# Performance work log

Hardware: AMD Instinct MI355X
Metric: run time of the kernel (lower is better)

## Reference

```python
import jax, jax.numpy as jnp
import numpy as np

NUM_HEADS = 16
HEAD_DIM = 64
D_MODEL = 1024
B, L = 8, 4096


def _relative_position_encoding(seq_len, dim):
    positions = jnp.arange(seq_len, dtype=jnp.float32)[:, None]
    div_term = jnp.exp(jnp.arange(0, dim, 2, dtype=jnp.float32) * (-(np.log(10000.0) / dim)))
    ang = positions * div_term  # [L, dim//2]
    pe = jnp.zeros((seq_len, dim), dtype=jnp.float32)
    pe = pe.at[:, 0::2].set(jnp.sin(ang))
    pe = pe.at[:, 1::2].set(jnp.cos(ang))
    return pe


def setup_inputs() -> dict:
    key = jax.random.key(0)
    k1, k2, k3 = jax.random.split(key, 3)
    x = jax.random.normal(k1, (B, L, D_MODEL), dtype=jnp.float32)
    w_qkv = jax.random.normal(k2, (D_MODEL, 3 * NUM_HEADS * HEAD_DIM), dtype=jnp.float32) * (1.0 / np.sqrt(D_MODEL))
    b_qkv = jnp.zeros((3 * NUM_HEADS * HEAD_DIM,), dtype=jnp.float32)
    w_out = jax.random.normal(k3, (NUM_HEADS * HEAD_DIM, D_MODEL), dtype=jnp.float32) * (1.0 / np.sqrt(NUM_HEADS * HEAD_DIM))
    b_out = jnp.zeros((D_MODEL,), dtype=jnp.float32)
    return {"x": x, "w_qkv": w_qkv, "b_qkv": b_qkv, "w_out": w_out, "b_out": b_out}


def reference(x, w_qkv, b_qkv, w_out, b_out):
    Bq, Lq, _ = x.shape
    qkv = x @ w_qkv + b_qkv                              # [B, L, 3*H*Dh]
    qkv = qkv.reshape(Bq, Lq, NUM_HEADS, 3 * HEAD_DIM)   # [B, L, H, 3*Dh]
    q, k, v = jnp.split(qkv, 3, axis=-1)                 # each [B, L, H, Dh]
    pos_enc = _relative_position_encoding(Lq, HEAD_DIM)  # [L, Dh]
    k = k + pos_enc[None, :, None, :]
    scale = jnp.sqrt(jnp.float32(HEAD_DIM))
    # NOTE: faithful to source -- contraction over head_dim with batch dims (B, L):
    # attention matrix is [B, L, H, H] (across heads, not sequence).
    attn = jnp.einsum('blhd,bl gd->blhg'.replace(' ', ''), q, k) / scale  # [B, L, H, H]
    attn = jax.nn.softmax(attn, axis=-1)
    out = jnp.einsum('blhg,blgd->blhd', attn, v)          # [B, L, H, Dh]
    out = out.reshape(Bq, Lq, NUM_HEADS * HEAD_DIM)
    return out @ w_out + b_out
```

## Files before the change

### kernel.cpp

```cpp
#include <hip/hip_runtime.h>
#include <hip/hip_bf16.h>
#include <cstdint>
#include <cstddef>

#define NH   16
#define DHD  64
#define DM   1024
#define BSZ  8
#define SEQ  4096
#define NTOK (BSZ*SEQ)
#define NQKV (3*NH*DHD)

typedef __attribute__((ext_vector_type(8))) __bf16 bf16x8;
typedef __attribute__((ext_vector_type(4))) float  floatx4;

static __device__ __forceinline__ unsigned short f2bf(float f) {
    unsigned int u = __float_as_uint(f);
    u += 0x7fffu + ((u >> 16) & 1u);
    return (unsigned short)(u >> 16);
}
static __device__ __forceinline__ float bf2f(unsigned int us) {
    return __uint_as_float(us << 16);
}
static __device__ __forceinline__ void load_lds16(const void* g, void* l) {
    __builtin_amdgcn_global_load_lds((__attribute__((address_space(1))) void*)g,
                                     (__attribute__((address_space(3))) void*)l,
                                     16, 0, 0);
}

__global__ __launch_bounds__(256) void k_cast_bf16(const float* __restrict__ in,
                                                   unsigned short* __restrict__ out, int n4) {
    int i = blockIdx.x * 256 + threadIdx.x;
    if (i >= n4) return;
    float4 v = ((const float4*)in)[i];
    ushort4 o;
    o.x = f2bf(v.x); o.y = f2bf(v.y); o.z = f2bf(v.z); o.w = f2bf(v.w);
    ((ushort4*)out)[i] = o;
}

template<int R, int C>
__global__ __launch_bounds__(256) void k_transpose_cast(const float* __restrict__ in,
                                                        unsigned short* __restrict__ out) {
    __shared__ float tile[32][33];
    int tx = threadIdx.x, ty = threadIdx.y;
    int col = blockIdx.x * 32 + tx;
#pragma unroll
    for (int k = 0; k < 4; k++) {
        int row = blockIdx.y * 32 + ty + k * 8;
        tile[ty + k * 8][tx] = in[(size_t)row * C + col];
    }
    __syncthreads();
#pragma unroll
    for (int k = 0; k < 4; k++) {
        int ocol = blockIdx.x * 32 + ty + k * 8;
        int orow = blockIdx.y * 32 + tx;
        out[(size_t)ocol * R + orow] = f2bf(tile[tx][ty + k * 8]);
    }
}

__global__ __launch_bounds__(256) void k_pe(float* __restrict__ pe) {
    int t = blockIdx.x * 256 + threadIdx.x;
    int l = t >> 5, i = t & 31;
    float dv = expf(-0.14391156831212787f * (float)(2 * i));
    float ang = (float)l * dv;
    pe[l * 64 + 2 * i]     = sinf(ang);
    pe[l * 64 + 2 * i + 1] = cosf(ang);
}

template<int N, int EPI>
__global__ __launch_bounds__(256) void k_gemm(const unsigned short* __restrict__ A,
                                              const unsigned short* __restrict__ BT,
                                              const float* __restrict__ bias,
                                              const float* __restrict__ pe,
                                              void* __restrict__ Cout) {
    constexpr int K = 1024;
    __shared__ __align__(16) short lds[8192];
    short* As = lds;
    short* Bs = lds + 4096;

    int tid  = threadIdx.x;
    int lane = tid & 63;
    int wid  = tid >> 6;
    int m0 = blockIdx.y * 128;
    int n0 = blockIdx.x * 128;
    int wr = wid >> 1, wc = wid & 1;
    int l15 = lane & 15;
    int kq  = (lane >> 4) * 8;

    floatx4 acc[4][4];
#pragma unroll
    for (int i = 0; i < 4; i++)
#pragma unroll
        for (int j = 0; j < 4; j++) acc[i][j] = (floatx4){0.f, 0.f, 0.f, 0.f};

    int ci0 = wid * 128 + lane;
    int ci1 = ci0 + 64;
    const unsigned short* pa0 = A  + (size_t)(m0 + (ci0 >> 2)) * K + (ci0 & 3) * 8;
    const unsigned short* pa1 = A  + (size_t)(m0 + (ci1 >> 2)) * K + (ci1 & 3) * 8;
    const unsigned short* pb0 = BT + (size_t)(n0 + (ci0 >> 2)) * K + (ci0 & 3) * 8;
    const unsigned short* pb1 = BT + (size_t)(n0 + (ci1 >> 2)) * K + (ci1 & 3) * 8;
    short* la0 = As + ci0 * 8;
    short* la1 = As + ci1 * 8;
    short* lb0 = Bs + ci0 * 8;
    short* lb1 = Bs + ci1 * 8;

    for (int kb = 0; kb < K; kb += 32) {
        __syncthreads();
        load_lds16(pa0 + kb, la0);
        load_lds16(pa1 + kb, la1);
        load_lds16(pb0 + kb, lb0);
        load_lds16(pb1 + kb, lb1);
        __syncthreads();

        bf16x8 aF[4], bF[4];
#pragma unroll
        for (int i = 0; i < 4; i++)
            aF[i] = *(const bf16x8*)&As[(wr * 64 + i * 16 + l15) * 32 + kq];
#pragma unroll
        for (int j = 0; j < 4; j++)
            bF[j] = *(const bf16x8*)&Bs[(wc * 64 + j * 16 + l15) * 32 + kq];
#pragma unroll
        for (int i = 0; i < 4; i++)
#pragma unroll
            for (int j = 0; j < 4; j++)
                acc[i][j] = __builtin_amdgcn_mfma_f32_16x16x32_bf16(aF[i], bF[j], acc[i][j], 0, 0, 0);
    }

    int rbase = (lane >> 4) * 4;
#pragma unroll
    for (int j = 0; j < 4; j++) {
        int col = n0 + wc * 64 + j * 16 + l15;
        float bv = bias[col];
        int h = 0, rc = 0;
        if (EPI == 1) { h = col / 192; rc = col - h * 192; }
#pragma unroll
        for (int i = 0; i < 4; i++) {
#pragma unroll
            for (int r = 0; r < 4; r++) {
                int row = m0 + wr * 64 + i * 16 + rbase + r;
                float v = acc[i][j][r] + bv;
                if (EPI == 1) {
                    if (rc < 64)        v *= 0.125f;
                    else if (rc < 128)  v += pe[(row & (SEQ - 1)) * 64 + (rc - 64)];
                    ((unsigned short*)Cout)[(size_t)row * N + col] = f2bf(v);
                } else {
                    ((float*)Cout)[(size_t)row * N + col] = v;
                }
            }
        }
    }
}

__global__ __launch_bounds__(256) void k_attn(const unsigned short* __restrict__ qkv,
                                              unsigned short* __restrict__ aout) {
    __shared__ __align__(16) float X4[4][3264];
    __shared__ float S4[4][272];
    int tid = threadIdx.x, wid = tid >> 6, lane = tid & 63;
    int t = blockIdx.x * 4 + wid;

    float* X = X4[wid];
    const unsigned short* src = qkv + (size_t)t * NQKV;

#pragma unroll
    for (int c = 0; c < 6; c++) {
        int ci = c * 64 + lane;
        uint4 u = ((const uint4*)src)[ci];
        int j0 = ci * 8;
        int h  = j0 / 192;
        int rc = j0 - h * 192;
        float* dst = X + h * 204 + rc;
        floatx4 f0 = { bf2f(u.x & 0xffff), bf2f(u.x >> 16), bf2f(u.y & 0xffff), bf2f(u.y >> 16) };
        floatx4 f1 = { bf2f(u.z & 0xffff), bf2f(u.z >> 16), bf2f(u.w & 0xffff), bf2f(u.w >> 16) };
        *(floatx4*)dst       = f0;
        *(floatx4*)(dst + 4) = f1;
    }
    __syncthreads();

    int h  = lane >> 2;
    int g0 = (lane & 3) * 4;
    const float* Q = X + h * 204;
    float s0 = 0.f, s1 = 0.f, s2 = 0.f, s3 = 0.f;
#pragma unroll 8
    for (int d = 0; d < 64; d++) {
        float qd = Q[d];
        s0 += qd * X[(g0 + 0) * 204 + 64 + d];
        s1 += qd * X[(g0 + 1) * 204 + 64 + d];
        s2 += qd * X[(g0 + 2) * 204 + 64 + d];
        s3 += qd * X[(g0 + 3) * 204 + 64 + d];
    }
    float mx = fmaxf(fmaxf(s0, s1), fmaxf(s2, s3));
    mx = fmaxf(mx, __shfl_xor(mx, 1));
    mx = fmaxf(mx, __shfl_xor(mx, 2));
    float e0 = __expf(s0 - mx), e1 = __expf(s1 - mx), e2 = __expf(s2 - mx), e3 = __expf(s3 - mx);
    float sum = e0 + e1 + e2 + e3;
    sum += __shfl_xor(sum, 1);
    sum += __shfl_xor(sum, 2);
    float inv = 1.0f / sum;
    float* Sr = &S4[wid][h * 17];
    Sr[g0 + 0] = e0 * inv; Sr[g0 + 1] = e1 * inv; Sr[g0 + 2] = e2 * inv; Sr[g0 + 3] = e3 * inv;
    __syncthreads();

    int db = lane & 3;
    floatx4 o0 = {0,0,0,0}, o1 = {0,0,0,0}, o2 = {0,0,0,0}, o3 = {0,0,0,0};
    const float* Sh = &S4[wid][h * 17];
#pragma unroll
    for (int g = 0; g < 16; g++) {
        float p = Sh[g];
        const floatx4* Vg = (const floatx4*)(X + g * 204 + 128 + db * 16);
        o0 += Vg[0] * p;
        o1 += Vg[1] * p;
        o2 += Vg[2] * p;
        o3 += Vg[3] * p;
    }
    unsigned int w[8];
    w[0] = (unsigned)f2bf(o0[0]) | ((unsigned)f2bf(o0[1]) << 16);
    w[1] = (unsigned)f2bf(o0[2]) | ((unsigned)f2bf(o0[3]) << 16);
    w[2] = (unsigned)f2bf(o1[0]) | ((unsigned)f2bf(o1[1]) << 16);
    w[3] = (unsigned)f2bf(o1[2]) | ((unsigned)f2bf(o1[3]) << 16);
    w[4] = (unsigned)f2bf(o2[0]) | ((unsigned)f2bf(o2[1]) << 16);
    w[5] = (unsigned)f2bf(o2[2]) | ((unsigned)f2bf(o2[3]) << 16);
    w[6] = (unsigned)f2bf(o3[0]) | ((unsigned)f2bf(o3[1]) << 16);
    w[7] = (unsigned)f2bf(o3[2]) | ((unsigned)f2bf(o3[3]) << 16);
    uint4* dst = (uint4*)&aout[(size_t)t * DM + h * 64 + db * 16];
    dst[0] = make_uint4(w[0], w[1], w[2], w[3]);
    dst[1] = make_uint4(w[4], w[5], w[6], w[7]);
}

extern "C" void kernel_launch(void* const* d_in, const int* in_sizes, int n_in,
                              void* d_out, int out_size, void* d_ws, size_t ws_size,
                              hipStream_t stream) {
    const float* x     = (const float*)d_in[0];
    const float* w_qkv = (const float*)d_in[1];
    const float* b_qkv = (const float*)d_in[2];
    const float* w_out = (const float*)d_in[3];
    const float* b_out = (const float*)d_in[4];
    float* out = (float*)d_out;

    char* ws = (char*)d_ws;
    float*          pe    = (float*)ws;
    unsigned short* wqkvT = (unsigned short*)(ws + (1u << 20));
    unsigned short* woutT = (unsigned short*)(ws + (1u << 20) + 6291456u);
    unsigned short* xbf   = (unsigned short*)(ws + (1u << 20) + 6291456u + 2097152u);
    unsigned short* qkv   = (unsigned short*)(ws + (1u << 20) + 6291456u + 2097152u + 67108864u);
    unsigned short* aout  = xbf;

    k_cast_bf16<<<(NTOK * DM / 4 + 255) / 256, 256, 0, stream>>>(x, xbf, NTOK * DM / 4);
    k_transpose_cast<1024, 3072><<<dim3(96, 32), dim3(32, 8), 0, stream>>>(w_qkv, wqkvT);
    k_transpose_cast<1024, 1024><<<dim3(32, 32), dim3(32, 8), 0, stream>>>(w_out, woutT);
    k_pe<<<512, 256, 0, stream>>>(pe);

    k_gemm<NQKV, 1><<<dim3(NQKV / 128, NTOK / 128), 256, 0, stream>>>(xbf, wqkvT, b_qkv, pe, qkv);

    k_attn<<<NTOK / 4, 256, 0, stream>>>(qkv, aout);

    k_gemm<DM, 0><<<dim3(DM / 128, NTOK / 128), 256, 0, stream>>>(aout, woutT, b_out, nullptr, out);
}
```

Measured before the change: 730.6 us.

## Replace GEMM with 256x256 8-wave pipelined MFMA kernel with swizzled LDS

Replaces the simple 128x128 single-buffered GEMM with a 256x256-tile, 512-thread kernel. It double-buffers K=64 tiles in LDS through async global-to-LDS loads interleaved with MFMA phases, and uses priority boosts and explicit waitcnt/barriers. It also adds an XOR-swizzled LDS layout against bank conflicts, an XCD-aware block-index remap, and an epilogue staged through LDS so global stores are vectorized. The goal is to hide memory latency and raise MFMA utilization in both projection GEMMs, at the cost of 128KB of LDS per block, fragile hand scheduling and lower occupancy.

```diff
diff --git a/kernel.cpp b/kernel.cpp
--- a/kernel.cpp
+++ b/kernel.cpp
@@ -68,84 +68,237 @@
 }
 
 template<int N, int EPI>
-__global__ __launch_bounds__(256) void k_gemm(const unsigned short* __restrict__ A,
-                                              const unsigned short* __restrict__ BT,
-                                              const float* __restrict__ bias,
-                                              const float* __restrict__ pe,
-                                              void* __restrict__ Cout) {
-    constexpr int K = 1024;
-    __shared__ __align__(16) short lds[8192];
-    short* As = lds;
-    short* Bs = lds + 4096;
-
-    int tid  = threadIdx.x;
-    int lane = tid & 63;
-    int wid  = tid >> 6;
-    int m0 = blockIdx.y * 128;
-    int n0 = blockIdx.x * 128;
-    int wr = wid >> 1, wc = wid & 1;
-    int l15 = lane & 15;
-    int kq  = (lane >> 4) * 8;
-
-    floatx4 acc[4][4];
-#pragma unroll
-    for (int i = 0; i < 4; i++)
-#pragma unroll
-        for (int j = 0; j < 4; j++) acc[i][j] = (floatx4){0.f, 0.f, 0.f, 0.f};
-
-    int ci0 = wid * 128 + lane;
-    int ci1 = ci0 + 64;
-    const unsigned short* pa0 = A  + (size_t)(m0 + (ci0 >> 2)) * K + (ci0 & 3) * 8;
-    const unsigned short* pa1 = A  + (size_t)(m0 + (ci1 >> 2)) * K + (ci1 & 3) * 8;
-    const unsigned short* pb0 = BT + (size_t)(n0 + (ci0 >> 2)) * K + (ci0 & 3) * 8;
-    const unsigned short* pb1 = BT + (size_t)(n0 + (ci1 >> 2)) * K + (ci1 & 3) * 8;
-    short* la0 = As + ci0 * 8;
-    short* la1 = As + ci1 * 8;
-    short* lb0 = Bs + ci0 * 8;
-    short* lb1 = Bs + ci1 * 8;
-
-    for (int kb = 0; kb < K; kb += 32) {
-        __syncthreads();
-        load_lds16(pa0 + kb, la0);
-        load_lds16(pa1 + kb, la1);
-        load_lds16(pb0 + kb, lb0);
-        load_lds16(pb1 + kb, lb1);
-        __syncthreads();
-
-        bf16x8 aF[4], bF[4];
-#pragma unroll
-        for (int i = 0; i < 4; i++)
-            aF[i] = *(const bf16x8*)&As[(wr * 64 + i * 16 + l15) * 32 + kq];
-#pragma unroll
-        for (int j = 0; j < 4; j++)
-            bF[j] = *(const bf16x8*)&Bs[(wc * 64 + j * 16 + l15) * 32 + kq];
-#pragma unroll
-        for (int i = 0; i < 4; i++)
-#pragma unroll
-            for (int j = 0; j < 4; j++)
-                acc[i][j] = __builtin_amdgcn_mfma_f32_16x16x32_bf16(aF[i], bF[j], acc[i][j], 0, 0, 0);
-    }
-
-    int rbase = (lane >> 4) * 4;
-#pragma unroll
-    for (int j = 0; j < 4; j++) {
-        int col = n0 + wc * 64 + j * 16 + l15;
-        float bv = bias[col];
-        int h = 0, rc = 0;
-        if (EPI == 1) { h = col / 192; rc = col - h * 192; }
-#pragma unroll
-        for (int i = 0; i < 4; i++) {
-#pragma unroll
-            for (int r = 0; r < 4; r++) {
-                int row = m0 + wr * 64 + i * 16 + rbase + r;
-                float v = acc[i][j][r] + bv;
-                if (EPI == 1) {
-                    if (rc < 64)        v *= 0.125f;
-                    else if (rc < 128)  v += pe[(row & (SEQ - 1)) * 64 + (rc - 64)];
-                    ((unsigned short*)Cout)[(size_t)row * N + col] = f2bf(v);
-                } else {
-                    ((float*)Cout)[(size_t)row * N + col] = v;
+__global__ __launch_bounds__(512, 2) void k_gemm8(const unsigned short* __restrict__ A,
+                                                  const unsigned short* __restrict__ BT,
+                                                  const float* __restrict__ bias,
+                                                  const float* __restrict__ pe,
+                                                  void* __restrict__ Cout) {
+    constexpr int K   = 1024;
+    constexpr int NKT = K / 64;
+    constexpr int NIT = NKT / 2;
+    constexpr int NBX = N / 256;
+    constexpr int nwg = NBX * (NTOK / 256);
+
+    __shared__ __align__(16) short sh[65536];
+    char* shb = (char*)sh;
+
+    const int tid  = threadIdx.x;
+    const int lane = tid & 63;
+    const int wid  = tid >> 6;
+    const int l15  = lane & 15;
+    const int q4   = lane >> 4;
+    const int wr   = wid >> 2;
+    const int wc   = wid & 3;
+
+    const int id = blockIdx.x;
+    const int sw = (id & 7) * (nwg >> 3) + (id >> 3);
+    const int m0 = (sw / NBX) * 256;
+    const int n0 = (sw % NBX) * 256;
+
+    int cj[2];
+    const unsigned short* srcA[2];
+    const unsigned short* srcB[2];
+#pragma unroll
+    for (int j = 0; j < 2; j++) {
+        int c  = wid * 128 + j * 64 + lane;
+        cj[j]  = c;
+        int rh = c >> 3;
+        int sl = (c & 7) ^ (rh & 7);
+        srcA[j] = A  + (size_t)(m0 + rh) * K + sl * 8;
+        srcB[j] = BT + (size_t)(n0 + rh) * K + sl * 8;
+    }
+    auto STAGE_A = [&](int kt, int half) {
+#pragma unroll
+        for (int j = 0; j < 2; j++)
+            load_lds16(srcA[j] + half * 128 * K + kt * 64,
+                       shb + (kt & 1) * 32768 + half * 16384 + cj[j] * 16);
+    };
+    auto STAGE_B = [&](int kt, int half) {
+#pragma unroll
+        for (int j = 0; j < 2; j++)
+            load_lds16(srcB[j] + half * 128 * K + kt * 64,
+                       shb + 65536 + (kt & 1) * 32768 + half * 16384 + cj[j] * 16);
+    };
+
+    const int swz  = (l15 & 7) << 4;
+    const int cb0  = ((q4 * 16) ^ swz);
+    const int cb1  = ((64 + q4 * 16) ^ swz);
+    const int rowA = (wr * 128 + l15) * 128;
+    const int rowB = (wc * 64  + l15) * 128;
+    auto RDA = [&](int b, int i, int cb) -> bf16x8 {
+        return *(const bf16x8*)(shb + b * 32768 + rowA + i * 2048 + cb);
+    };
+    auto RDB = [&](int b, int n, int cb) -> bf16x8 {
+        return *(const bf16x8*)(shb + 65536 + b * 32768 + rowB + n * 2048 + cb);
+    };
+
+    floatx4 acc[8][4];
+#pragma unroll
+    for (int i = 0; i < 8; i++)
+#pragma unroll
+        for (int n = 0; n < 4; n++) acc[i][n] = (floatx4){0.f, 0.f, 0.f, 0.f};
+
+    bf16x8 aF0[4][2], aF1[4][2], bF[4][2];
+
+    STAGE_A(0, 0); STAGE_B(0, 0); STAGE_A(0, 1); STAGE_B(0, 1);
+    STAGE_A(1, 0); STAGE_B(1, 0);
+    asm volatile("s_waitcnt vmcnt(4)" ::: "memory");
+    __builtin_amdgcn_s_barrier();
+
+#pragma unroll 1
+    for (int it = 0; it < NIT; ++it) {
+        const int kB = 2 * it + 1;
+        const bool more = (it < NIT - 1);
+
+#pragma unroll
+        for (int i = 0; i < 4; i++) { aF0[i][0] = RDA(0, i, cb0); aF0[i][1] = RDA(0, i, cb1); }
+#pragma unroll
+        for (int n = 0; n < 4; n++) bF[n][0] = RDB(0, n, cb0);
+        STAGE_A(kB, 1);
+        __builtin_amdgcn_s_barrier();
+        asm volatile("s_waitcnt lgkmcnt(0)" ::: "memory");
+        __builtin_amdgcn_s_setprio(1);
+#pragma unroll
+        for (int i = 0; i < 4; i++)
+#pragma unroll
+            for (int n = 0; n < 4; n++)
+                acc[i][n] = __builtin_amdgcn_mfma_f32_16x16x32_bf16(aF0[i][0], bF[n][0], acc[i][n], 0, 0, 0);
+        __builtin_amdgcn_s_setprio(0);
+        __builtin_amdgcn_s_barrier();
+
+#pragma unroll
+        for (int i = 0; i < 4; i++) { aF1[i][0] = RDA(0, i + 4, cb0); aF1[i][1] = RDA(0, i + 4, cb1); }
+#pragma unroll
+        for (int n = 0; n < 4; n++) bF[n][1] = RDB(0, n, cb1);
+        STAGE_B(kB, 1);
+        __builtin_amdgcn_s_barrier();
+        asm volatile("s_waitcnt lgkmcnt(0)" ::: "memory");
+        __builtin_amdgcn_s_setprio(1);
+#pragma unroll
+        for (int i = 0; i < 4; i++)
+#pragma unroll
+            for (int n = 0; n < 4; n++)
+                acc[i][n] = __builtin_amdgcn_mfma_f32_16x16x32_bf16(aF0[i][1], bF[n][1], acc[i][n], 0, 0, 0);
+        __builtin_amdgcn_s_setprio(0);
+        __builtin_amdgcn_s_barrier();
+
+        if (more) STAGE_A(kB + 1, 0);
+        __builtin_amdgcn_s_barrier();
+        __builtin_amdgcn_s_setprio(1);
+#pragma unroll
+        for (int i = 0; i < 4; i++)
+#pragma unroll
+            for (int n = 0; n < 4; n++)
+                acc[i + 4][n] = __builtin_amdgcn_mfma_f32_16x16x32_bf16(aF1[i][0], bF[n][0], acc[i + 4][n], 0, 0, 0);
+        __builtin_amdgcn_s_setprio(0);
+        __builtin_amdgcn_s_barrier();
+
+        if (more) STAGE_B(kB + 1, 0);
+        if (more) asm volatile("s_waitcnt vmcnt(4)" ::: "memory");
+        else      asm volatile("s_waitcnt vmcnt(0)" ::: "memory");
+        __builtin_amdgcn_s_barrier();
+        __builtin_amdgcn_s_setprio(1);
+#pragma unroll
+        for (int i = 0; i < 4; i++)
+#pragma unroll
+            for (int n = 0; n < 4; n++)
+                acc[i + 4][n] = __builtin_amdgcn_mfma_f32_16x16x32_bf16(aF1[i][1], bF[n][1], acc[i + 4][n], 0, 0, 0);
+        __builtin_amdgcn_s_setprio(0);
+        __builtin_amdgcn_s_barrier();
+
+#pragma unroll
+        for (int i = 0; i < 4; i++) { aF0[i][0] = RDA(1, i, cb0); aF0[i][1] = RDA(1, i, cb1); }
+#pragma unroll
+        for (int n = 0; n < 4; n++) bF[n][0] = RDB(1, n, cb0);
+        if (more) STAGE_A(kB + 1, 1);
+        __builtin_amdgcn_s_barrier();
+        asm volatile("s_waitcnt lgkmcnt(0)" ::: "memory");
+        __builtin_amdgcn_s_setprio(1);
+#pragma unroll
+        for (int i = 0; i < 4; i++)
+#pragma unroll
+            for (int n = 0; n < 4; n++)
+                acc[i][n] = __builtin_amdgcn_mfma_f32_16x16x32_bf16(aF0[i][0], bF[n][0], acc[i][n], 0, 0, 0);
+        __builtin_amdgcn_s_setprio(0);
+        __builtin_amdgcn_s_barrier();
+
+#pragma unroll
+        for (int i = 0; i < 4; i++) { aF1[i][0] = RDA(1, i + 4, cb0); aF1[i][1] = RDA(1, i + 4, cb1); }
+#pragma unroll
+        for (int n = 0; n < 4; n++) bF[n][1] = RDB(1, n, cb1);
+        if (more) STAGE_B(kB + 1, 1);
+        __builtin_amdgcn_s_barrier();
+        asm volatile("s_waitcnt lgkmcnt(0)" ::: "memory");
+        __builtin_amdgcn_s_setprio(1);
+#pragma unroll
+        for (int i = 0; i < 4; i++)
+#pragma unroll
+            for (int n = 0; n < 4; n++)
+                acc[i][n] = __builtin_amdgcn_mfma_f32_16x16x32_bf16(aF0[i][1], bF[n][1], acc[i][n], 0, 0, 0);
+        __builtin_amdgcn_s_setprio(0);
+        __builtin_amdgcn_s_barrier();
+
+        if (more) STAGE_A(kB + 2, 0);
+        __builtin_amdgcn_s_barrier();
+        __builtin_amdgcn_s_setprio(1);
+#pragma unroll
+        for (int i = 0; i < 4; i++)
+#pragma unroll
+            for (int n = 0; n < 4; n++)
+                acc[i + 4][n] = __builtin_amdgcn_mfma_f32_16x16x32_bf16(aF1[i][0], bF[n][0], acc[i + 4][n], 0, 0, 0);
+        __builtin_amdgcn_s_setprio(0);
+        __builtin_amdgcn_s_barrier();
+
+        if (more) STAGE_B(kB + 2, 0);
+        if (more) asm volatile("s_waitcnt vmcnt(4)" ::: "memory");
+        __builtin_amdgcn_s_barrier();
+        __builtin_amdgcn_s_setprio(1);
+#pragma unroll
+        for (int i = 0; i < 4; i++)
+#pragma unroll
+            for (int n = 0; n < 4; n++)
+                acc[i + 4][n] = __builtin_amdgcn_mfma_f32_16x16x32_bf16(aF1[i][1], bF[n][1], acc[i + 4][n], 0, 0, 0);
+        __builtin_amdgcn_s_setprio(0);
+        __builtin_amdgcn_s_barrier();
+    }
+
+    float* X = (float*)shb + wid * 2176;
+#pragma unroll
+    for (int cidx = 0; cidx < 4; ++cidx) {
+#pragma unroll
+        for (int i2 = 0; i2 < 2; ++i2) {
+            const int i = cidx * 2 + i2;
+#pragma unroll
+            for (int n = 0; n < 4; ++n) {
+                const int col = n0 + wc * 64 + n * 16 + l15;
+                const float bv = bias[col];
+                int rc = 0;
+                if (EPI == 1) { int h = col / 192; rc = col - h * 192; }
+#pragma unroll
+                for (int r = 0; r < 4; ++r) {
+                    const int lrow = i2 * 16 + q4 * 4 + r;
+                    float v = acc[i][n][r] + bv;
+                    if (EPI == 1) {
+                        const int grow = m0 + wr * 128 + cidx * 32 + lrow;
+                        if (rc < 64)        v *= 0.125f;
+                        else if (rc < 128)  v += pe[(grow & (SEQ - 1)) * 64 + (rc - 64)];
+                    }
+                    X[lrow * 68 + n * 16 + l15] = v;
                 }
+            }
+        }
+#pragma unroll
+        for (int rr = 0; rr < 8; ++rr) {
+            const int lr   = rr * 4 + q4;
+            const int grow = m0 + wr * 128 + cidx * 32 + lr;
+            const float* p = X + lr * 68 + l15 * 4;
+            if (EPI == 1) {
+                ushort4 o;
+                o.x = f2bf(p[0]); o.y = f2bf(p[1]); o.z = f2bf(p[2]); o.w = f2bf(p[3]);
+                *(ushort4*)((unsigned short*)Cout + (size_t)grow * N + n0 + wc * 64 + l15 * 4) = o;
+            } else {
+                float4 o = make_float4(p[0], p[1], p[2], p[3]);
+                *(float4*)((float*)Cout + (size_t)grow * N + n0 + wc * 64 + l15 * 4) = o;
             }
         }
     }
@@ -249,9 +402,9 @@
     k_transpose_cast<1024, 1024><<<dim3(32, 32), dim3(32, 8), 0, stream>>>(w_out, woutT);
     k_pe<<<512, 256, 0, stream>>>(pe);
 
-    k_gemm<NQKV, 1><<<dim3(NQKV / 128, NTOK / 128), 256, 0, stream>>>(xbf, wqkvT, b_qkv, pe, qkv);
+    k_gemm8<NQKV, 1><<<dim3((NQKV / 256) * (NTOK / 256)), 512, 0, stream>>>(xbf, wqkvT, b_qkv, pe, qkv);
 
     k_attn<<<NTOK / 4, 256, 0, stream>>>(qkv, aout);
 
-    k_gemm<DM, 0><<<dim3(DM / 128, NTOK / 128), 256, 0, stream>>>(aout, woutT, b_out, nullptr, out);
-}
+    k_gemm8<DM, 0><<<dim3((DM / 256) * (NTOK / 256)), 512, 0, stream>>>(aout, woutT, b_out, nullptr, out);
+}
```

Measured after the change: 874.5 us. 1.2x slower.

## Deepen GEMM K-tile to 64 with XOR-swizzled LDS and staged coalesced epilogue

Applied to the files above, without the earlier changes.

The bf16 MFMA GEMM now stages 64-wide K slices per iteration, halving the number of barrier pairs, and applies an XOR swizzle to the LDS layout to avoid bank conflicts on fragment reads. The epilogue writes accumulators through a per-wave LDS staging buffer so each lane stores 4 contiguous outputs as vector stores instead of scattered scalar stores. This doubles the LDS footprint to 32KB, which may reduce occupancy, and adds an extra barrier and LDS round trip in the epilogue.

```diff
diff --git a/kernel.cpp b/kernel.cpp
--- a/kernel.cpp
+++ b/kernel.cpp
@@ -74,18 +74,17 @@
                                               const float* __restrict__ pe,
                                               void* __restrict__ Cout) {
     constexpr int K = 1024;
-    __shared__ __align__(16) short lds[8192];
-    short* As = lds;
-    short* Bs = lds + 4096;
-
-    int tid  = threadIdx.x;
-    int lane = tid & 63;
-    int wid  = tid >> 6;
-    int m0 = blockIdx.y * 128;
-    int n0 = blockIdx.x * 128;
-    int wr = wid >> 1, wc = wid & 1;
-    int l15 = lane & 15;
-    int kq  = (lane >> 4) * 8;
+    __shared__ __align__(16) short lds[16384];
+    char* shb = (char*)lds;
+
+    const int tid  = threadIdx.x;
+    const int lane = tid & 63;
+    const int wid  = tid >> 6;
+    const int l15  = lane & 15;
+    const int q4   = lane >> 4;
+    const int m0 = blockIdx.y * 128;
+    const int n0 = blockIdx.x * 128;
+    const int wr = wid >> 1, wc = wid & 1;
 
     floatx4 acc[4][4];
 #pragma unroll
@@ -93,59 +92,87 @@
 #pragma unroll
         for (int j = 0; j < 4; j++) acc[i][j] = (floatx4){0.f, 0.f, 0.f, 0.f};
 
-    int ci0 = wid * 128 + lane;
-    int ci1 = ci0 + 64;
-    const unsigned short* pa0 = A  + (size_t)(m0 + (ci0 >> 2)) * K + (ci0 & 3) * 8;
-    const unsigned short* pa1 = A  + (size_t)(m0 + (ci1 >> 2)) * K + (ci1 & 3) * 8;
-    const unsigned short* pb0 = BT + (size_t)(n0 + (ci0 >> 2)) * K + (ci0 & 3) * 8;
-    const unsigned short* pb1 = BT + (size_t)(n0 + (ci1 >> 2)) * K + (ci1 & 3) * 8;
-    short* la0 = As + ci0 * 8;
-    short* la1 = As + ci1 * 8;
-    short* lb0 = Bs + ci0 * 8;
-    short* lb1 = Bs + ci1 * 8;
-
-    for (int kb = 0; kb < K; kb += 32) {
+    const int ci0 = wid * 256 + lane;
+    const int rh0 = ci0 >> 3;
+    const int sl  = (lane & 7) ^ ((lane >> 3) & 7);
+    const unsigned short* srcA = A  + (size_t)(m0 + rh0) * K + sl * 8;
+    const unsigned short* srcB = BT + (size_t)(n0 + rh0) * K + sl * 8;
+    char* dstA = shb + ci0 * 16;
+    char* dstB = shb + 16384 + ci0 * 16;
+
+    const int swz  = (l15 & 7) << 4;
+    const int cb0  = (q4 * 16) ^ swz;
+    const int rowA = (wr * 64 + l15) * 128;
+    const int rowB = (wc * 64 + l15) * 128;
+
+    for (int kb = 0; kb < K; kb += 64) {
         __syncthreads();
-        load_lds16(pa0 + kb, la0);
-        load_lds16(pa1 + kb, la1);
-        load_lds16(pb0 + kb, lb0);
-        load_lds16(pb1 + kb, lb1);
+#pragma unroll
+        for (int j = 0; j < 4; j++) {
+            load_lds16(srcA + kb + j * 8 * K, dstA + j * 1024);
+            load_lds16(srcB + kb + j * 8 * K, dstB + j * 1024);
+        }
         __syncthreads();
 
         bf16x8 aF[4], bF[4];
 #pragma unroll
         for (int i = 0; i < 4; i++)
-            aF[i] = *(const bf16x8*)&As[(wr * 64 + i * 16 + l15) * 32 + kq];
+            aF[i] = *(const bf16x8*)(shb + rowA + i * 2048 + cb0);
 #pragma unroll
         for (int j = 0; j < 4; j++)
-            bF[j] = *(const bf16x8*)&Bs[(wc * 64 + j * 16 + l15) * 32 + kq];
+            bF[j] = *(const bf16x8*)(shb + 16384 + rowB + j * 2048 + cb0);
 #pragma unroll
         for (int i = 0; i < 4; i++)
 #pragma unroll
             for (int j = 0; j < 4; j++)
                 acc[i][j] = __builtin_amdgcn_mfma_f32_16x16x32_bf16(aF[i], bF[j], acc[i][j], 0, 0, 0);
-    }
-
-    int rbase = (lane >> 4) * 4;
-#pragma unroll
-    for (int j = 0; j < 4; j++) {
-        int col = n0 + wc * 64 + j * 16 + l15;
-        float bv = bias[col];
-        int h = 0, rc = 0;
-        if (EPI == 1) { h = col / 192; rc = col - h * 192; }
-#pragma unroll
-        for (int i = 0; i < 4; i++) {
-#pragma unroll
-            for (int r = 0; r < 4; r++) {
-                int row = m0 + wr * 64 + i * 16 + rbase + r;
-                float v = acc[i][j][r] + bv;
+#pragma unroll
+        for (int i = 0; i < 4; i++)
+            aF[i] = *(const bf16x8*)(shb + rowA + i * 2048 + (cb0 ^ 64));
+#pragma unroll
+        for (int j = 0; j < 4; j++)
+            bF[j] = *(const bf16x8*)(shb + 16384 + rowB + j * 2048 + (cb0 ^ 64));
+#pragma unroll
+        for (int i = 0; i < 4; i++)
+#pragma unroll
+            for (int j = 0; j < 4; j++)
+                acc[i][j] = __builtin_amdgcn_mfma_f32_16x16x32_bf16(aF[i], bF[j], acc[i][j], 0, 0, 0);
+    }
+
+    __syncthreads();
+    float* X = (float*)shb + wid * 1088;
+#pragma unroll
+    for (int i = 0; i < 4; ++i) {
+#pragma unroll
+        for (int n = 0; n < 4; ++n) {
+            const int col = n0 + wc * 64 + n * 16 + l15;
+            const float bv = bias[col];
+            int rc = 0;
+            if (EPI == 1) { int h = col / 192; rc = col - h * 192; }
+#pragma unroll
+            for (int r = 0; r < 4; ++r) {
+                const int lrow = q4 * 4 + r;
+                float v = acc[i][n][r] + bv;
                 if (EPI == 1) {
+                    const int grow = m0 + wr * 64 + i * 16 + lrow;
                     if (rc < 64)        v *= 0.125f;
-                    else if (rc < 128)  v += pe[(row & (SEQ - 1)) * 64 + (rc - 64)];
-                    ((unsigned short*)Cout)[(size_t)row * N + col] = f2bf(v);
-                } else {
-                    ((float*)Cout)[(size_t)row * N + col] = v;
+                    else if (rc < 128)  v += pe[(grow & (SEQ - 1)) * 64 + (rc - 64)];
                 }
+                X[lrow * 68 + n * 16 + l15] = v;
+            }
+        }
+#pragma unroll
+        for (int rr = 0; rr < 4; ++rr) {
+            const int lr   = rr * 4 + q4;
+            const int grow = m0 + wr * 64 + i * 16 + lr;
+            const float* p = X + lr * 68 + l15 * 4;
+            if (EPI == 1) {
+                ushort4 o;
+                o.x = f2bf(p[0]); o.y = f2bf(p[1]); o.z = f2bf(p[2]); o.w = f2bf(p[3]);
+                *(ushort4*)((unsigned short*)Cout + (size_t)grow * N + n0 + wc * 64 + l15 * 4) = o;
+            } else {
+                float4 o = make_float4(p[0], p[1], p[2], p[3]);
+                *(float4*)((float*)Cout + (size_t)grow * N + n0 + wc * 64 + l15 * 4) = o;
             }
         }
     }
```

Measured after the change: 776.0 us. 6.2% more time.

## Compute cross-head attention with bf16 MFMA instead of scalar FP32 LDS loops

Applied to the files above, without the earlier changes.

Rewrites the per-token attention kernel so that Q·K^T and P·V each use 16x16x32 bf16 MFMA instructions. Q and K fragments are loaded straight from global memory in bf16, replacing the old path that unpacked everything to fp32 in LDS and ran scalar dot products. Softmax is done in registers with 16-lane shuffles, and only V and the bf16 probabilities are staged in a small per-wave LDS buffer. This cuts LDS footprint and ALU work, but rounds the probabilities to bf16 and drops block-level barriers, relying on the fact that each wave only touches its own LDS region.

```diff
diff --git a/kernel.cpp b/kernel.cpp
--- a/kernel.cpp
+++ b/kernel.cpp
@@ -153,77 +153,86 @@
 
 __global__ __launch_bounds__(256) void k_attn(const unsigned short* __restrict__ qkv,
                                               unsigned short* __restrict__ aout) {
-    __shared__ __align__(16) float X4[4][3264];
-    __shared__ float S4[4][272];
-    int tid = threadIdx.x, wid = tid >> 6, lane = tid & 63;
-    int t = blockIdx.x * 4 + wid;
-
-    float* X = X4[wid];
+    __shared__ __align__(16) unsigned short VB[4][16 * 72];
+    __shared__ __align__(16) unsigned short PB[4][16 * 16];
+    const int tid = threadIdx.x, wid = tid >> 6, lane = tid & 63;
+    const int l15 = lane & 15, q4 = lane >> 4;
+    const int t = blockIdx.x * 4 + wid;
     const unsigned short* src = qkv + (size_t)t * NQKV;
 
-#pragma unroll
-    for (int c = 0; c < 6; c++) {
-        int ci = c * 64 + lane;
-        uint4 u = ((const uint4*)src)[ci];
-        int j0 = ci * 8;
-        int h  = j0 / 192;
-        int rc = j0 - h * 192;
-        float* dst = X + h * 204 + rc;
-        floatx4 f0 = { bf2f(u.x & 0xffff), bf2f(u.x >> 16), bf2f(u.y & 0xffff), bf2f(u.y >> 16) };
-        floatx4 f1 = { bf2f(u.z & 0xffff), bf2f(u.z >> 16), bf2f(u.w & 0xffff), bf2f(u.w >> 16) };
-        *(floatx4*)dst       = f0;
-        *(floatx4*)(dst + 4) = f1;
-    }
-    __syncthreads();
-
-    int h  = lane >> 2;
-    int g0 = (lane & 3) * 4;
-    const float* Q = X + h * 204;
-    float s0 = 0.f, s1 = 0.f, s2 = 0.f, s3 = 0.f;
-#pragma unroll 8
-    for (int d = 0; d < 64; d++) {
-        float qd = Q[d];
-        s0 += qd * X[(g0 + 0) * 204 + 64 + d];
-        s1 += qd * X[(g0 + 1) * 204 + 64 + d];
-        s2 += qd * X[(g0 + 2) * 204 + 64 + d];
-        s3 += qd * X[(g0 + 3) * 204 + 64 + d];
-    }
-    float mx = fmaxf(fmaxf(s0, s1), fmaxf(s2, s3));
-    mx = fmaxf(mx, __shfl_xor(mx, 1));
-    mx = fmaxf(mx, __shfl_xor(mx, 2));
-    float e0 = __expf(s0 - mx), e1 = __expf(s1 - mx), e2 = __expf(s2 - mx), e3 = __expf(s3 - mx);
-    float sum = e0 + e1 + e2 + e3;
-    sum += __shfl_xor(sum, 1);
-    sum += __shfl_xor(sum, 2);
-    float inv = 1.0f / sum;
-    float* Sr = &S4[wid][h * 17];
-    Sr[g0 + 0] = e0 * inv; Sr[g0 + 1] = e1 * inv; Sr[g0 + 2] = e2 * inv; Sr[g0 + 3] = e3 * inv;
-    __syncthreads();
-
-    int db = lane & 3;
-    floatx4 o0 = {0,0,0,0}, o1 = {0,0,0,0}, o2 = {0,0,0,0}, o3 = {0,0,0,0};
-    const float* Sh = &S4[wid][h * 17];
-#pragma unroll
-    for (int g = 0; g < 16; g++) {
-        float p = Sh[g];
-        const floatx4* Vg = (const floatx4*)(X + g * 204 + 128 + db * 16);
-        o0 += Vg[0] * p;
-        o1 += Vg[1] * p;
-        o2 += Vg[2] * p;
-        o3 += Vg[3] * p;
-    }
-    unsigned int w[8];
-    w[0] = (unsigned)f2bf(o0[0]) | ((unsigned)f2bf(o0[1]) << 16);
-    w[1] = (unsigned)f2bf(o0[2]) | ((unsigned)f2bf(o0[3]) << 16);
-    w[2] = (unsigned)f2bf(o1[0]) | ((unsigned)f2bf(o1[1]) << 16);
-    w[3] = (unsigned)f2bf(o1[2]) | ((unsigned)f2bf(o1[3]) << 16);
-    w[4] = (unsigned)f2bf(o2[0]) | ((unsigned)f2bf(o2[1]) << 16);
-    w[5] = (unsigned)f2bf(o2[2]) | ((unsigned)f2bf(o2[3]) << 16);
-    w[6] = (unsigned)f2bf(o3[0]) | ((unsigned)f2bf(o3[1]) << 16);
-    w[7] = (unsigned)f2bf(o3[2]) | ((unsigned)f2bf(o3[3]) << 16);
-    uint4* dst = (uint4*)&aout[(size_t)t * DM + h * 64 + db * 16];
-    dst[0] = make_uint4(w[0], w[1], w[2], w[3]);
-    dst[1] = make_uint4(w[4], w[5], w[6], w[7]);
+    unsigned short* vb = VB[wid];
+    unsigned short* pb = PB[wid];
+
+    {
+        const int g = lane >> 2, seg = lane & 3;
+        const unsigned short* vsrc = src + g * 192 + 128 + seg * 16;
+        uint4 v0 = *(const uint4*)(vsrc);
+        uint4 v1 = *(const uint4*)(vsrc + 8);
+        *(uint4*)(vb + g * 72 + seg * 16)     = v0;
+        *(uint4*)(vb + g * 72 + seg * 16 + 8) = v1;
+    }
+
+    bf16x8 qf0 = *(const bf16x8*)(src + l15 * 192 +       q4 * 8);
+    bf16x8 qf1 = *(const bf16x8*)(src + l15 * 192 + 32  + q4 * 8);
+    bf16x8 kf0 = *(const bf16x8*)(src + l15 * 192 + 64  + q4 * 8);
+    bf16x8 kf1 = *(const bf16x8*)(src + l15 * 192 + 96  + q4 * 8);
+
+    floatx4 s = (floatx4){0.f, 0.f, 0.f, 0.f};
+    s = __builtin_amdgcn_mfma_f32_16x16x32_bf16(qf0, kf0, s, 0, 0, 0);
+    s = __builtin_amdgcn_mfma_f32_16x16x32_bf16(qf1, kf1, s, 0, 0, 0);
+
+#pragma unroll
+    for (int r = 0; r < 4; r++) {
+        float v = s[r];
+        float mx = v;
+        mx = fmaxf(mx, __shfl_xor(mx, 1));
+        mx = fmaxf(mx, __shfl_xor(mx, 2));
+        mx = fmaxf(mx, __shfl_xor(mx, 4));
+        mx = fmaxf(mx, __shfl_xor(mx, 8));
+        float e = __expf(v - mx);
+        float sm = e;
+        sm += __shfl_xor(sm, 1);
+        sm += __shfl_xor(sm, 2);
+        sm += __shfl_xor(sm, 4);
+        sm += __shfl_xor(sm, 8);
+        float p = e * (1.0f / sm);
+        pb[(q4 * 4 + r) * 16 + l15] = f2bf(p);
+    }
+
+    bf16x8 pA = *(const bf16x8*)(pb + l15 * 16 + (q4 & 1) * 8);
+
+    union VFrag { bf16x8 v; unsigned short u[8]; };
+    floatx4 o[4];
+#pragma unroll
+    for (int db = 0; db < 4; db++) o[db] = (floatx4){0.f, 0.f, 0.f, 0.f};
+
+#pragma unroll
+    for (int db = 0; db < 4; db++) {
+        VFrag vf;
+#pragma unroll
+        for (int e = 0; e < 8; e++) vf.u[e] = 0;
+        if (q4 < 2) {
+#pragma unroll
+            for (int e = 0; e < 8; e++)
+                vf.u[e] = vb[(q4 * 8 + e) * 72 + db * 16 + l15];
+        }
+        o[db] = __builtin_amdgcn_mfma_f32_16x16x32_bf16(pA, vf.v, o[db], 0, 0, 0);
+    }
+
+#pragma unroll
+    for (int db = 0; db < 4; db++)
+#pragma unroll
+        for (int r = 0; r < 4; r++)
+            vb[(q4 * 4 + r) * 72 + db * 16 + l15] = f2bf(o[db][r]);
+
+    {
+        const int row = lane >> 2, seg = lane & 3;
+        uint4 w0 = *(const uint4*)(vb + row * 72 + seg * 16);
+        uint4 w1 = *(const uint4*)(vb + row * 72 + seg * 16 + 8);
+        uint4* dst = (uint4*)&aout[(size_t)t * DM + row * 64 + seg * 16];
+        dst[0] = w0;
+        dst[1] = w1;
+    }
 }
 
 extern "C" void kernel_launch(void* const* d_in, const int* in_sizes, int n_in,
```

After: 705.7 us. 1.04x faster.
